# Optimization experiments

Hardware: AMD Instinct MI355X
Metric: run time of the kernel (lower is better)

Reference implementation:

```python
import jax, jax.numpy as jnp
import numpy as np

D_MODEL = 256
D_HIDDEN = 1024
B, S = 4, 32768


def setup_inputs() -> dict:
    key = jax.random.key(0)
    k_x, k_m, k_w1, k_b1, k_w2, k_b2 = jax.random.split(key, 6)
    x = jax.random.normal(k_x, (B, S, D_MODEL), dtype=jnp.float32)
    # graph_dependency: binary connectivity mask [d_hidden, d_model]
    mask = jax.random.randint(k_m, (D_HIDDEN, D_MODEL), 0, 2, dtype=jnp.int32)
    lim1 = 1.0 / np.sqrt(D_MODEL)
    lim2 = 1.0 / np.sqrt(D_HIDDEN)
    w1 = jax.random.uniform(k_w1, (D_HIDDEN, D_MODEL), jnp.float32, -lim1, lim1)
    b1 = jax.random.uniform(k_b1, (D_HIDDEN,), jnp.float32, -lim1, lim1)
    # reserve=True: maps d_hidden -> d_model with transposed mask
    w2 = jax.random.uniform(k_w2, (D_MODEL, D_HIDDEN), jnp.float32, -lim2, lim2)
    b2 = jax.random.uniform(k_b2, (D_MODEL,), jnp.float32, -lim2, lim2)
    return {"x": x, "w1": w1, "b1": b1, "w2": w2, "b2": b2, "mask": mask}


def reference(x, w1, b1, w2, b2, mask):
    m = mask.astype(x.dtype)                      # [H, D]
    # fc1: graph-masked linear d_model -> d_hidden
    h = jnp.einsum('bsd,hd->bsh', x, w1 * m) + b1  # [B, S, H]
    h = jax.nn.relu(h)
    # fc2 (reserve): graph-masked linear d_hidden -> d_model, transposed mask
    y = jnp.einsum('bsh,dh->bsd', h, w2 * m.T) + b2  # [B, S, D]
    return y
```

## Files before the change

### kernel.cpp

```cpp
#include <hip/hip_runtime.h>


#define D_MODEL 256
#define D_HID   1024
#define MT      128
#define NPHASE  16
#define SUBC_ELEMS 8192

typedef __attribute__((ext_vector_type(8))) short short8;
typedef __attribute__((ext_vector_type(16))) float f32x16;
typedef __attribute__((ext_vector_type(4))) unsigned int uint4v;

__device__ __forceinline__ unsigned short f2bf(float f) {
  union { float f; unsigned int u; } v; v.f = f;
  unsigned int u = v.u;
  return (unsigned short)((u + 0x7FFFu + ((u >> 16) & 1u)) >> 16);
}

__device__ __forceinline__ unsigned cvtpk_bf16(float lo, float hi) {
  unsigned r;
  asm("v_cvt_pk_bf16_f32 %0, %1, %2" : "=v"(r) : "v"(lo), "v"(hi));
  return r;
}

__device__ __forceinline__ void plswap(unsigned &a, unsigned &b) {
  asm("v_permlane32_swap_b32 %0, %1" : "+v"(a), "+v"(b));
}

__device__ __forceinline__ void async16(void* lds, const void* g) {
  __builtin_amdgcn_global_load_lds(
      (const __attribute__((address_space(1))) unsigned int*)g,
      (__attribute__((address_space(3))) unsigned int*)lds,
      16, 0, 0);
}

__global__ __launch_bounds__(256) void prep_weights(
    const float* __restrict__ w1, const float* __restrict__ w2,
    const int* __restrict__ mask,
    unsigned short* __restrict__ W1p, unsigned short* __restrict__ W2p)
{
  int t = blockIdx.x * 256 + threadIdx.x;
  if (t < 32768) {
    int c    = t >> 10;
    int kf   = (t >> 6) & 15;
    int lane = t & 63;
    int h = c * 32 + (lane & 31);
    int k = kf * 16 + (lane >> 5) * 8;
    const float* wp = w1 + h * 256 + k;
    const int*   mp = mask + h * 256 + k;
    short8 v;
    #pragma unroll
    for (int j = 0; j < 8; ++j) v[j] = (short)(mp[j] ? f2bf(wp[j]) : 0);
    *(short8*)(W1p + (size_t)t * 8) = v;
  } else {
    int s    = t - 32768;
    int c    = s >> 10;
    int cf   = (s >> 7) & 7;
    int kf2  = (s >> 6) & 1;
    int lane = s & 63;
    int n = cf * 32 + (lane & 31);
    int h = c * 32 + kf2 * 16 + (lane >> 5) * 8;
    short8 v;
    #pragma unroll
    for (int j = 0; j < 8; ++j)
      v[j] = (short)(mask[(h + j) * 256 + n] ? f2bf(w2[n * 1024 + h + j]) : 0);
    *(short8*)(W2p + (size_t)s * 8) = v;
  }
}

__global__ __launch_bounds__(256, 2) void ffd_fused(
    const float* __restrict__ X, const float* __restrict__ b1,
    const float* __restrict__ b2,
    const unsigned short* __restrict__ W1p, const unsigned short* __restrict__ W2p,
    float* __restrict__ Y)
{
  __shared__ unsigned short sW1[2 * SUBC_ELEMS];
  __shared__ unsigned short sW2[2 * SUBC_ELEMS];
  __shared__ float sB1[D_HID];

  const int tid  = threadIdx.x;
  const int lane = tid & 63;
  const int w    = tid >> 6;
  const int l32  = lane & 31;
  const int q2   = lane >> 5;

  const long rowBase = (long)blockIdx.x * MT + w * 32;

  short8 xf[16];
  const float* xrow = X + (rowBase + l32) * D_MODEL;
  #pragma unroll
  for (int kf = 0; kf < 16; ++kf) {
    const float4 f0 = *(const float4*)(xrow + kf * 16 + q2 * 8);
    const float4 f1 = *(const float4*)(xrow + kf * 16 + q2 * 8 + 4);
    short8 v;
    v[0] = (short)f2bf(f0.x); v[1] = (short)f2bf(f0.y);
    v[2] = (short)f2bf(f0.z); v[3] = (short)f2bf(f0.w);
    v[4] = (short)f2bf(f1.x); v[5] = (short)f2bf(f1.y);
    v[6] = (short)f2bf(f1.z); v[7] = (short)f2bf(f1.w);
    xf[kf] = v;
  }

  f32x16 acc[8];
  #pragma unroll
  for (int i = 0; i < 8; ++i)
    #pragma unroll
    for (int j = 0; j < 16; ++j) acc[i][j] = 0.f;

  async16(&sB1[tid * 4], b1 + tid * 4);

  for (int C = 0; C < NPHASE; ++C) {
    __syncthreads();
    {
      const unsigned short* g1 = W1p + (size_t)C * (2 * SUBC_ELEMS) + tid * 8;
      const unsigned short* g2 = W2p + (size_t)C * (2 * SUBC_ELEMS) + tid * 8;
      unsigned short* d1 = &sW1[tid * 8];
      unsigned short* d2 = &sW2[tid * 8];
      #pragma unroll
      for (int i = 0; i < 8; ++i) {
        async16(d1 + i * 2048, g1 + i * 2048);
        async16(d2 + i * 2048, g2 + i * 2048);
      }
    }
    __syncthreads();

    #pragma unroll
    for (int p = 0; p < 2; ++p) {
      const int c = C * 2 + p;
      const unsigned short* w1c = &sW1[p * SUBC_ELEMS];
      const unsigned short* w2c = &sW2[p * SUBC_ELEMS];

      float4 bb[4];
      #pragma unroll
      for (int g = 0; g < 4; ++g)
        bb[g] = *(const float4*)&sB1[c * 32 + 4 * q2 + 8 * g];

      f32x16 h0, h1;
      #pragma unroll
      for (int j = 0; j < 16; ++j) { h0[j] = 0.f; h1[j] = 0.f; }
      __builtin_amdgcn_s_setprio(1);
      #pragma unroll
      for (int kf = 0; kf < 8; ++kf) {
        short8 wa = *(const short8*)&w1c[kf * 512 + lane * 8];
        short8 wb = *(const short8*)&w1c[(kf + 8) * 512 + lane * 8];
        h0 = __builtin_amdgcn_mfma_f32_32x32x16_bf16(wa, xf[kf],     h0, 0, 0, 0);
        h1 = __builtin_amdgcn_mfma_f32_32x32x16_bf16(wb, xf[kf + 8], h1, 0, 0, 0);
      }
      __builtin_amdgcn_s_setprio(0);

      float v[16];
      #pragma unroll
      for (int r = 0; r < 16; ++r) {
        float t = h0[r] + h1[r] + bb[r >> 2][r & 3];
        v[r] = t > 0.f ? t : 0.f;
      }

      unsigned W0 = cvtpk_bf16(v[0],  v[1]),  W1 = cvtpk_bf16(v[2],  v[3]);
      unsigned W2 = cvtpk_bf16(v[4],  v[5]),  W3 = cvtpk_bf16(v[6],  v[7]);
      unsigned W4 = cvtpk_bf16(v[8],  v[9]),  W5 = cvtpk_bf16(v[10], v[11]);
      unsigned W6 = cvtpk_bf16(v[12], v[13]), W7 = cvtpk_bf16(v[14], v[15]);
      plswap(W0, W2); plswap(W1, W3); plswap(W4, W6); plswap(W5, W7);
      union { uint4v u; short8 s; } A0, A1;
      A0.u = (uint4v){W0, W1, W2, W3};
      A1.u = (uint4v){W4, W5, W6, W7};

      __builtin_amdgcn_s_setprio(1);
      #pragma unroll
      for (int cf = 0; cf < 8; ++cf) {
        short8 b0  = *(const short8*)&w2c[(cf * 2 + 0) * 512 + lane * 8];
        short8 b1f = *(const short8*)&w2c[(cf * 2 + 1) * 512 + lane * 8];
        acc[cf] = __builtin_amdgcn_mfma_f32_32x32x16_bf16(A0.s, b0,  acc[cf], 0, 0, 0);
        acc[cf] = __builtin_amdgcn_mfma_f32_32x32x16_bf16(A1.s, b1f, acc[cf], 0, 0, 0);
      }
      __builtin_amdgcn_s_setprio(0);
    }
  }

  #pragma unroll
  for (int cf = 0; cf < 8; ++cf) {
    int col = cf * 32 + l32;
    float bias = b2[col];
    #pragma unroll
    for (int r = 0; r < 16; ++r) {
      long row = rowBase + (r & 3) + 8 * (r >> 2) + 4 * q2;
      Y[row * D_MODEL + col] = acc[cf][r] + bias;
    }
  }
}

extern "C" void kernel_launch(void* const* d_in, const int* in_sizes, int n_in,
                              void* d_out, int out_size, void* d_ws, size_t ws_size,
                              hipStream_t stream) {
  const float* x    = (const float*)d_in[0];
  const float* w1   = (const float*)d_in[1];
  const float* b1   = (const float*)d_in[2];
  const float* w2   = (const float*)d_in[3];
  const float* b2   = (const float*)d_in[4];
  const int*   mask = (const int*)d_in[5];

  unsigned short* W1p = (unsigned short*)d_ws;
  unsigned short* W2p = W1p + (size_t)D_HID * D_MODEL;
  float* Y = (float*)d_out;

  prep_weights<<<256, 256, 0, stream>>>(w1, w2, mask, W1p, W2p);
  ffd_fused<<<131072 / MT, 256, 0, stream>>>(x, b1, b2, W1p, W2p, Y);
}
```

Before: 160.0 us.

## Interleave fc2 MFMAs of sub-chunk A with fc1 MFMAs of sub-chunk B

Unrolls the two sub-chunks of each phase by hand and software-pipelines them. The fc1 GEMM of the second sub-chunk is interleaved with the fc2 GEMM of the first, so independent MFMA chains alternate. This hides the dependency latency of the serialized accumulator chains and the bias/ReLU/pack step between the two GEMMs. It raises register pressure, since h0/h1 and the A0/A1 fragments are live together, which could cause spills under the 2-waves launch bound.

Result: slower. 221.8 us (+38.6%).

```diff
diff --git a/kernel.cpp b/kernel.cpp
--- a/kernel.cpp
+++ b/kernel.cpp
@@ -123,56 +123,91 @@
     }
     __syncthreads();
 
-    #pragma unroll
-    for (int p = 0; p < 2; ++p) {
-      const int c = C * 2 + p;
-      const unsigned short* w1c = &sW1[p * SUBC_ELEMS];
-      const unsigned short* w2c = &sW2[p * SUBC_ELEMS];
-
+    const unsigned short* w1A = &sW1[0];
+    const unsigned short* w2A = &sW2[0];
+    const unsigned short* w1B = &sW1[SUBC_ELEMS];
+    const unsigned short* w2B = &sW2[SUBC_ELEMS];
+    const int cA = C * 2, cB = C * 2 + 1;
+
+    f32x16 h0, h1;
+    #pragma unroll
+    for (int j = 0; j < 16; ++j) { h0[j] = 0.f; h1[j] = 0.f; }
+    __builtin_amdgcn_s_setprio(1);
+    #pragma unroll
+    for (int kf = 0; kf < 8; ++kf) {
+      short8 wa = *(const short8*)&w1A[kf * 512 + lane * 8];
+      short8 wb = *(const short8*)&w1A[(kf + 8) * 512 + lane * 8];
+      h0 = __builtin_amdgcn_mfma_f32_32x32x16_bf16(wa, xf[kf],     h0, 0, 0, 0);
+      h1 = __builtin_amdgcn_mfma_f32_32x32x16_bf16(wb, xf[kf + 8], h1, 0, 0, 0);
+    }
+    __builtin_amdgcn_s_setprio(0);
+
+    union { uint4v u; short8 s; } A0, A1;
+    {
       float4 bb[4];
       #pragma unroll
       for (int g = 0; g < 4; ++g)
-        bb[g] = *(const float4*)&sB1[c * 32 + 4 * q2 + 8 * g];
-
-      f32x16 h0, h1;
-      #pragma unroll
-      for (int j = 0; j < 16; ++j) { h0[j] = 0.f; h1[j] = 0.f; }
-      __builtin_amdgcn_s_setprio(1);
-      #pragma unroll
-      for (int kf = 0; kf < 8; ++kf) {
-        short8 wa = *(const short8*)&w1c[kf * 512 + lane * 8];
-        short8 wb = *(const short8*)&w1c[(kf + 8) * 512 + lane * 8];
-        h0 = __builtin_amdgcn_mfma_f32_32x32x16_bf16(wa, xf[kf],     h0, 0, 0, 0);
-        h1 = __builtin_amdgcn_mfma_f32_32x32x16_bf16(wb, xf[kf + 8], h1, 0, 0, 0);
-      }
-      __builtin_amdgcn_s_setprio(0);
-
+        bb[g] = *(const float4*)&sB1[cA * 32 + 4 * q2 + 8 * g];
       float v[16];
       #pragma unroll
       for (int r = 0; r < 16; ++r) {
         float t = h0[r] + h1[r] + bb[r >> 2][r & 3];
         v[r] = t > 0.f ? t : 0.f;
       }
-
       unsigned W0 = cvtpk_bf16(v[0],  v[1]),  W1 = cvtpk_bf16(v[2],  v[3]);
       unsigned W2 = cvtpk_bf16(v[4],  v[5]),  W3 = cvtpk_bf16(v[6],  v[7]);
       unsigned W4 = cvtpk_bf16(v[8],  v[9]),  W5 = cvtpk_bf16(v[10], v[11]);
       unsigned W6 = cvtpk_bf16(v[12], v[13]), W7 = cvtpk_bf16(v[14], v[15]);
       plswap(W0, W2); plswap(W1, W3); plswap(W4, W6); plswap(W5, W7);
-      union { uint4v u; short8 s; } A0, A1;
       A0.u = (uint4v){W0, W1, W2, W3};
       A1.u = (uint4v){W4, W5, W6, W7};
-
-      __builtin_amdgcn_s_setprio(1);
-      #pragma unroll
-      for (int cf = 0; cf < 8; ++cf) {
-        short8 b0  = *(const short8*)&w2c[(cf * 2 + 0) * 512 + lane * 8];
-        short8 b1f = *(const short8*)&w2c[(cf * 2 + 1) * 512 + lane * 8];
-        acc[cf] = __builtin_amdgcn_mfma_f32_32x32x16_bf16(A0.s, b0,  acc[cf], 0, 0, 0);
-        acc[cf] = __builtin_amdgcn_mfma_f32_32x32x16_bf16(A1.s, b1f, acc[cf], 0, 0, 0);
+    }
+
+    #pragma unroll
+    for (int j = 0; j < 16; ++j) { h0[j] = 0.f; h1[j] = 0.f; }
+    __builtin_amdgcn_s_setprio(1);
+    #pragma unroll
+    for (int i = 0; i < 8; ++i) {
+      short8 b0  = *(const short8*)&w2A[(i * 2 + 0) * 512 + lane * 8];
+      short8 b1f = *(const short8*)&w2A[(i * 2 + 1) * 512 + lane * 8];
+      short8 wa  = *(const short8*)&w1B[i * 512 + lane * 8];
+      short8 wb  = *(const short8*)&w1B[(i + 8) * 512 + lane * 8];
+      acc[i] = __builtin_amdgcn_mfma_f32_32x32x16_bf16(A0.s, b0,  acc[i], 0, 0, 0);
+      h0 = __builtin_amdgcn_mfma_f32_32x32x16_bf16(wa, xf[i],     h0, 0, 0, 0);
+      acc[i] = __builtin_amdgcn_mfma_f32_32x32x16_bf16(A1.s, b1f, acc[i], 0, 0, 0);
+      h1 = __builtin_amdgcn_mfma_f32_32x32x16_bf16(wb, xf[i + 8], h1, 0, 0, 0);
+    }
+    __builtin_amdgcn_s_setprio(0);
+
+    {
+      float4 bb[4];
+      #pragma unroll
+      for (int g = 0; g < 4; ++g)
+        bb[g] = *(const float4*)&sB1[cB * 32 + 4 * q2 + 8 * g];
+      float v[16];
+      #pragma unroll
+      for (int r = 0; r < 16; ++r) {
+        float t = h0[r] + h1[r] + bb[r >> 2][r & 3];
+        v[r] = t > 0.f ? t : 0.f;
       }
-      __builtin_amdgcn_s_setprio(0);
-    }
+      unsigned W0 = cvtpk_bf16(v[0],  v[1]),  W1 = cvtpk_bf16(v[2],  v[3]);
+      unsigned W2 = cvtpk_bf16(v[4],  v[5]),  W3 = cvtpk_bf16(v[6],  v[7]);
+      unsigned W4 = cvtpk_bf16(v[8],  v[9]),  W5 = cvtpk_bf16(v[10], v[11]);
+      unsigned W6 = cvtpk_bf16(v[12], v[13]), W7 = cvtpk_bf16(v[14], v[15]);
+      plswap(W0, W2); plswap(W1, W3); plswap(W4, W6); plswap(W5, W7);
+      A0.u = (uint4v){W0, W1, W2, W3};
+      A1.u = (uint4v){W4, W5, W6, W7};
+    }
+
+    __builtin_amdgcn_s_setprio(1);
+    #pragma unroll
+    for (int cf = 0; cf < 8; ++cf) {
+      short8 b0  = *(const short8*)&w2B[(cf * 2 + 0) * 512 + lane * 8];
+      short8 b1f = *(const short8*)&w2B[(cf * 2 + 1) * 512 + lane * 8];
+      acc[cf] = __builtin_amdgcn_mfma_f32_32x32x16_bf16(A0.s, b0,  acc[cf], 0, 0, 0);
+      acc[cf] = __builtin_amdgcn_mfma_f32_32x32x16_bf16(A1.s, b1f, acc[cf], 0, 0, 0);
+    }
+    __builtin_amdgcn_s_setprio(0);
   }
 
   #pragma unroll
```
